# Kernel tuning notes

Hardware: AMD Instinct MI355X
Metric: run time of the kernel (lower is better)

The kernel has to match this reference:

```python
import jax, jax.numpy as jnp
import numpy as np

B, T, C, H = 4, 2048, 1024, 16
D = C // H  # head_size = 64


def _layernorm(x, g, b, eps=1e-5):
    mu = jnp.mean(x, axis=-1, keepdims=True)
    var = jnp.var(x, axis=-1, keepdims=True)
    return (x - mu) * jax.lax.rsqrt(var + eps) * g + b


def setup_inputs() -> dict:
    key = jax.random.key(0)
    ks = jax.random.split(key, 12)
    s = 0.02
    return {
        "x": jax.random.normal(ks[0], (B, T, C), dtype=jnp.float32),
        "Wq": jax.random.normal(ks[1], (C, C), dtype=jnp.float32) * s,
        "Wk": jax.random.normal(ks[2], (C, C), dtype=jnp.float32) * s,
        "Wv": jax.random.normal(ks[3], (C, C), dtype=jnp.float32) * s,
        "Wo": jax.random.normal(ks[4], (C, C), dtype=jnp.float32) * s,
        "bo": jnp.zeros((C,), dtype=jnp.float32),
        "ln1_g": jnp.ones((C,), dtype=jnp.float32),
        "ln1_b": jnp.zeros((C,), dtype=jnp.float32),
        "ln2_g": jnp.ones((C,), dtype=jnp.float32),
        "ln2_b": jnp.zeros((C,), dtype=jnp.float32),
        "W1": jax.random.normal(ks[5], (C, 4 * C), dtype=jnp.float32) * s,
        "b1": jnp.zeros((4 * C,), dtype=jnp.float32),
        "W2": jax.random.normal(ks[6], (4 * C, C), dtype=jnp.float32) * s,
        "b2": jnp.zeros((C,), dtype=jnp.float32),
    }


def reference(x, Wq, Wk, Wv, Wo, bo, ln1_g, ln1_b, ln2_g, ln2_b, W1, b1, W2, b2):
    # --- self-attention branch (pre-LN) ---
    h = _layernorm(x, ln1_g, ln1_b)
    q = (h @ Wq).reshape(B, T, H, D)
    k = (h @ Wk).reshape(B, T, H, D)
    v = (h @ Wv).reshape(B, T, H, D)
    scores = jnp.einsum("bqhd,bkhd->bhqk", q, k) * (D ** -0.5)
    causal = jnp.tril(jnp.ones((T, T), dtype=bool))
    scores = jnp.where(causal, scores, -jnp.inf)
    attn = jax.nn.softmax(scores, axis=-1)  # dropout=0 in eval
    out = jnp.einsum("bhqk,bkhd->bqhd", attn, v).reshape(B, T, C)
    x = x + (out @ Wo + bo)
    # --- feed-forward branch (pre-LN) ---
    h2 = _layernorm(x, ln2_g, ln2_b)
    ff = jax.nn.relu(h2 @ W1 + b1) @ W2 + b2
    return x + ff
```

## Files before the change

kernel.cpp:

```cpp
#include <hip/hip_runtime.h>
#include <hip/hip_bf16.h>
#include <math.h>

#define Bsz 4
#define Tsz 2048
#define Csz 1024
#define Hsz 16
#define Dsz 64
#define Msz (Bsz * Tsz)

typedef __attribute__((ext_vector_type(8))) __bf16 bf16x8;
typedef __attribute__((ext_vector_type(2))) __bf16 bf16x2;
typedef __attribute__((ext_vector_type(4))) float f32x4;

#define GLOBAL_AS __attribute__((address_space(1)))
#define LDS_AS    __attribute__((address_space(3)))


__device__ __forceinline__ float block_sum256(float v, float* sh) {
#pragma unroll
    for (int o = 32; o > 0; o >>= 1) v += __shfl_down(v, o, 64);
    int lane = threadIdx.x & 63, w = threadIdx.x >> 6;
    __syncthreads();
    if (lane == 0) sh[w] = v;
    __syncthreads();
    return sh[0] + sh[1] + sh[2] + sh[3];
}


__global__ __launch_bounds__(256) void layernorm_bf16(const float* __restrict__ x,
                                                      const float* __restrict__ g,
                                                      const float* __restrict__ b,
                                                      __bf16* __restrict__ out) {
    __shared__ float sh[4];
    const int row = blockIdx.x;
    const float* xr = x + (size_t)row * Csz;
    float v[4];
    float s = 0.f, ss = 0.f;
#pragma unroll
    for (int i = 0; i < 4; i++) {
        v[i] = xr[threadIdx.x + i * 256];
        s += v[i];
        ss += v[i] * v[i];
    }
    float tot = block_sum256(s, sh);
    float mean = tot * (1.0f / Csz);
    float tot2 = block_sum256(ss, sh);
    float var = tot2 * (1.0f / Csz) - mean * mean;
    float inv = rsqrtf(var + 1e-5f);
    __bf16* orow = out + (size_t)row * Csz;
#pragma unroll
    for (int i = 0; i < 4; i++) {
        int c = threadIdx.x + i * 256;
        orow[c] = (__bf16)((v[i] - mean) * inv * g[c] + b[c]);
    }
}


__global__ __launch_bounds__(256) void transpose_bf16(const float* __restrict__ W,
                                                      __bf16* __restrict__ Wt,
                                                      int K, int N) {
    __shared__ float t[32][33];
    const int k0 = blockIdx.y * 32, n0 = blockIdx.x * 32;
    const int c = threadIdx.x & 31, r8 = threadIdx.x >> 5;
#pragma unroll
    for (int it = 0; it < 4; it++) {
        int r = r8 + it * 8;
        t[r][c] = W[(size_t)(k0 + r) * N + n0 + c];
    }
    __syncthreads();
#pragma unroll
    for (int it = 0; it < 4; it++) {
        int r = r8 + it * 8;
        Wt[(size_t)(n0 + r) * K + k0 + c] = (__bf16)t[c][r];
    }
}

__global__ __launch_bounds__(256) void transpose4_bf16(const float* __restrict__ Wa,
                                                       const float* __restrict__ Wb,
                                                       const float* __restrict__ Wc,
                                                       const float* __restrict__ Wd,
                                                       __bf16* __restrict__ Ta,
                                                       __bf16* __restrict__ Tb,
                                                       __bf16* __restrict__ Tc,
                                                       __bf16* __restrict__ Td) {
    __shared__ float t[32][33];
    const float* W = (blockIdx.z == 0) ? Wa : (blockIdx.z == 1) ? Wb : (blockIdx.z == 2) ? Wc : Wd;
    __bf16* Wt = (blockIdx.z == 0) ? Ta : (blockIdx.z == 1) ? Tb : (blockIdx.z == 2) ? Tc : Td;
    const int k0 = blockIdx.y * 32, n0 = blockIdx.x * 32;
    const int c = threadIdx.x & 31, r8 = threadIdx.x >> 5;
#pragma unroll
    for (int it = 0; it < 4; it++) {
        int r = r8 + it * 8;
        t[r][c] = W[(size_t)(k0 + r) * Csz + n0 + c];
    }
    __syncthreads();
#pragma unroll
    for (int it = 0; it < 4; it++) {
        int r = r8 + it * 8;
        Wt[(size_t)(n0 + r) * Csz + k0 + c] = (__bf16)t[c][r];
    }
}


__global__ __launch_bounds__(256) void gemm_bf16(const __bf16* __restrict__ A,
                                                 const __bf16* __restrict__ Bt,
                                                 float* __restrict__ Cf,
                                                 float* __restrict__ Cf2,
                                                 __bf16* __restrict__ Cb,
                                                 int M, int N, int K, int ld,
                                                 const float* __restrict__ bias,
                                                 const float* __restrict__ resid,
                                                 int do_relu) {
    __shared__ __bf16 As[128 * 64];
    __shared__ __bf16 Bs[128 * 64];

    const int tid = threadIdx.x;
    const int lane = tid & 63;
    const int w = tid >> 6;
    const int rowBase = blockIdx.y * 128;
    const int colBase = blockIdx.x * 128;
    const int wr = (w & 1) * 64;
    const int wc = (w >> 1) * 64;

    const __bf16* Ak = A + (size_t)blockIdx.z * K;
    const __bf16* Bk = Bt + (size_t)blockIdx.z * K;
    float* Cfu = Cf;
    const float* residu = resid;
    const float* biasu = bias;
    if (blockIdx.z == 1) { Cfu = Cf2; residu = nullptr; biasu = nullptr; }

    const int m16 = lane & 15;
    const int kg = lane >> 4;
    const int swz = m16 & 7;

    const int sr = lane >> 3;
    const int sc = lane & 7;
    const int gcs = sc ^ sr;

    f32x4 acc[4][4] = {};

    for (int k0 = 0; k0 < K; k0 += 64) {
        __syncthreads();
#pragma unroll
        for (int it = 0; it < 4; it++) {
            int lr = w * 32 + it * 8;
            const __bf16* ga = Ak + (size_t)(rowBase + lr + sr) * ld + k0 + gcs * 8;
            __builtin_amdgcn_global_load_lds((const GLOBAL_AS unsigned int*)ga,
                                             (LDS_AS unsigned int*)(As + lr * 64),
                                             16, 0, 0);
            const __bf16* gb = Bk + (size_t)(colBase + lr + sr) * ld + k0 + gcs * 8;
            __builtin_amdgcn_global_load_lds((const GLOBAL_AS unsigned int*)gb,
                                             (LDS_AS unsigned int*)(Bs + lr * 64),
                                             16, 0, 0);
        }
        __syncthreads();

#pragma unroll
        for (int s = 0; s < 2; s++) {
            const int slot = ((s * 4 + kg) ^ swz) * 8;
            bf16x8 af[4], bfv[4];
#pragma unroll
            for (int i = 0; i < 4; i++)
                af[i] = *(const bf16x8*)(As + (wr + i * 16 + m16) * 64 + slot);
#pragma unroll
            for (int j = 0; j < 4; j++)
                bfv[j] = *(const bf16x8*)(Bs + (wc + j * 16 + m16) * 64 + slot);
#pragma unroll
            for (int i = 0; i < 4; i++)
#pragma unroll
                for (int j = 0; j < 4; j++)
                    acc[i][j] = __builtin_amdgcn_mfma_f32_16x16x32_bf16(af[i], bfv[j], acc[i][j], 0, 0, 0);
        }
    }

    const int cn = lane & 15;
    const int rq = (lane >> 4) * 4;
    float bj[4];
#pragma unroll
    for (int j = 0; j < 4; j++)
        bj[j] = biasu ? biasu[colBase + wc + j * 16 + cn] : 0.f;

#pragma unroll
    for (int i = 0; i < 4; i++) {
#pragma unroll
        for (int r = 0; r < 4; r++) {
            int m = rowBase + wr + i * 16 + rq + r;
            size_t rowOff = (size_t)m * N;
#pragma unroll
            for (int j = 0; j < 4; j++) {
                int n = colBase + wc + j * 16 + cn;
                float v = acc[i][j][r] + bj[j];
                if (do_relu) v = fmaxf(v, 0.f);
                if (residu) v += residu[rowOff + n];
                if (Cfu) Cfu[rowOff + n] = v;
                if (Cb && blockIdx.z == 0) Cb[rowOff + n] = (__bf16)v;
            }
        }
    }
}


__global__ __launch_bounds__(256) void add_partial(float* __restrict__ out,
                                                   const float* __restrict__ p,
                                                   const float* __restrict__ b2) {
    size_t i = ((size_t)blockIdx.x * 256 + threadIdx.x) * 4;
    float4 o = *(float4*)(out + i);
    const float4 a = *(const float4*)(p + i);
    const float4 bb = *(const float4*)(b2 + (i & (Csz - 1)));
    o.x += a.x + bb.x;
    o.y += a.y + bb.y;
    o.z += a.z + bb.z;
    o.w += a.w + bb.w;
    *(float4*)(out + i) = o;
}


__global__ __launch_bounds__(256, 4) void attn_mfma(const __bf16* __restrict__ QKV,
                                                    __bf16* __restrict__ O) {
    __shared__ __bf16 Ks[64 * 64];
    __shared__ __bf16 Vt[64 * 72];
    __shared__ __bf16 Ps[128 * 72];

    const int tid = threadIdx.x;
    const int lane = tid & 63;
    const int w = tid >> 6;
    const int bh = blockIdx.x;
    const int b = bh >> 4, h = bh & 15;
    const int qt = (int)gridDim.y - 1 - (int)blockIdx.y;
    const int qbase = qt * 128;
    const int ld3C = 3 * Csz;

    const __bf16* Qg = QKV + (size_t)(b * Tsz) * ld3C + h * Dsz;
    const __bf16* Kg = Qg + Csz;
    const __bf16* Vg = Qg + 2 * Csz;

    const int m16 = lane & 15;
    const int kg = lane >> 4;
    const int rq = kg * 4;
    const int wrow = w * 32;
    const int swz = m16 & 7;

    bf16x8 aq[2][2];
#pragma unroll
    for (int i = 0; i < 2; i++)
#pragma unroll
        for (int s = 0; s < 2; s++)
            aq[i][s] = *(const bf16x8*)(Qg + (size_t)(qbase + wrow + i * 16 + m16) * ld3C + (s * 4 + kg) * 8);

    const int sr = lane >> 3;
    const int sc = lane & 7;
    const int gcs = sc ^ sr;

    const int kp = (lane & 31) * 2;
    const int dg = w * 2 + (lane >> 5);

    f32x4 Oacc[2][4];
    float l_part[2][4];
#pragma unroll
    for (int i = 0; i < 2; i++)
#pragma unroll
        for (int j = 0; j < 4; j++) Oacc[i][j] = (f32x4){0.f, 0.f, 0.f, 0.f};
#pragma unroll
    for (int i = 0; i < 2; i++)
#pragma unroll
        for (int r = 0; r < 4; r++) l_part[i][r] = 0.f;

    const float CEXP = 0.18033688f;

    const int nkt = 2 * qt + 2;
    for (int kt = 0; kt < nkt; kt++) {
        const int kbase = kt * 64;
        __syncthreads();

#pragma unroll
        for (int it = 0; it < 2; it++) {
            int lr = w * 16 + it * 8 + sr;
            const __bf16* src = Kg + (size_t)(kbase + lr) * ld3C + gcs * 8;
            __builtin_amdgcn_global_load_lds((const GLOBAL_AS unsigned int*)src,
                                             (LDS_AS unsigned int*)(Ks + (w * 16 + it * 8) * 64),
                                             16, 0, 0);
        }
        bf16x8 v0 = *(const bf16x8*)(Vg + (size_t)(kbase + kp) * ld3C + dg * 8);
        bf16x8 v1 = *(const bf16x8*)(Vg + (size_t)(kbase + kp + 1) * ld3C + dg * 8);
        __syncthreads();

        f32x4 S[2][4];
#pragma unroll
        for (int i = 0; i < 2; i++)
#pragma unroll
            for (int j = 0; j < 4; j++) S[i][j] = (f32x4){0.f, 0.f, 0.f, 0.f};
#pragma unroll
        for (int s = 0; s < 2; s++) {
            bf16x8 bk[4];
#pragma unroll
            for (int j = 0; j < 4; j++)
                bk[j] = *(const bf16x8*)(Ks + (j * 16 + m16) * 64 + (((s * 4 + kg) ^ swz) * 8));
#pragma unroll
            for (int i = 0; i < 2; i++)
#pragma unroll
                for (int j = 0; j < 4; j++)
                    S[i][j] = __builtin_amdgcn_mfma_f32_16x16x32_bf16(aq[i][s], bk[j], S[i][j], 0, 0, 0);
        }

        const bool domask = (kt >= 2 * qt);
#pragma unroll
        for (int i = 0; i < 2; i++) {
#pragma unroll
            for (int j = 0; j < 4; j++) {
#pragma unroll
                for (int r = 0; r < 4; r++) {
                    float arg = S[i][j][r] * CEXP;
                    if (domask && (kbase + j * 16 + m16 > qbase + wrow + i * 16 + rq + r))
                        arg = -INFINITY;
                    float e = exp2f(arg);
                    S[i][j][r] = e;
                    l_part[i][r] += e;
                }
            }
        }

#pragma unroll
        for (int i = 0; i < 2; i++)
#pragma unroll
            for (int j = 0; j < 4; j++)
#pragma unroll
                for (int r = 0; r < 4; r++)
                    Ps[(wrow + i * 16 + rq + r) * 72 + j * 16 + m16] = (__bf16)S[i][j][r];
#pragma unroll
        for (int e = 0; e < 8; e++) {
            bf16x2 pr;
            pr[0] = v0[e];
            pr[1] = v1[e];
            *(bf16x2*)(Vt + (dg * 8 + e) * 72 + kp) = pr;
        }
        __syncthreads();

#pragma unroll
        for (int s = 0; s < 2; s++) {
            bf16x8 ap[2], bv[4];
#pragma unroll
            for (int i = 0; i < 2; i++)
                ap[i] = *(const bf16x8*)(Ps + (wrow + i * 16 + m16) * 72 + s * 32 + kg * 8);
#pragma unroll
            for (int j = 0; j < 4; j++)
                bv[j] = *(const bf16x8*)(Vt + (j * 16 + m16) * 72 + s * 32 + kg * 8);
#pragma unroll
            for (int i = 0; i < 2; i++)
#pragma unroll
                for (int j = 0; j < 4; j++)
                    Oacc[i][j] = __builtin_amdgcn_mfma_f32_16x16x32_bf16(ap[i], bv[j], Oacc[i][j], 0, 0, 0);
        }
    }

#pragma unroll
    for (int i = 0; i < 2; i++) {
#pragma unroll
        for (int r = 0; r < 4; r++) {
            float l = l_part[i][r];
#pragma unroll
            for (int msk = 1; msk < 16; msk <<= 1) l += __shfl_xor(l, msk, 64);
            const float inv = 1.0f / l;
            const int qrow = qbase + wrow + i * 16 + rq + r;
            __bf16* orow = O + (size_t)(b * Tsz + qrow) * Csz + h * Dsz;
#pragma unroll
            for (int j = 0; j < 4; j++)
                orow[j * 16 + m16] = (__bf16)(Oacc[i][j][r] * inv);
        }
    }
}


extern "C" void kernel_launch(void* const* d_in, const int* in_sizes, int n_in,
                              void* d_out, int out_size, void* d_ws, size_t ws_size,
                              hipStream_t stream) {
    const float* x     = (const float*)d_in[0];
    const float* Wq    = (const float*)d_in[1];
    const float* Wk    = (const float*)d_in[2];
    const float* Wv    = (const float*)d_in[3];
    const float* Wo    = (const float*)d_in[4];
    const float* bo    = (const float*)d_in[5];
    const float* ln1_g = (const float*)d_in[6];
    const float* ln1_b = (const float*)d_in[7];
    const float* ln2_g = (const float*)d_in[8];
    const float* ln2_b = (const float*)d_in[9];
    const float* W1    = (const float*)d_in[10];
    const float* b1    = (const float*)d_in[11];
    const float* W2    = (const float*)d_in[12];
    const float* b2    = (const float*)d_in[13];
    float* out = (float*)d_out;

    const size_t MB = 1u << 20;
    char* w = (char*)d_ws;
    __bf16* h    = (__bf16*)(w + 0);
    __bf16* Wqkv = (__bf16*)(w + 16 * MB);
    __bf16* Wot  = (__bf16*)(w + 22 * MB);
    __bf16* W1t  = (__bf16*)(w + 24 * MB);
    __bf16* W2t  = (__bf16*)(w + 32 * MB);
    __bf16* QKVb = (__bf16*)(w + 40 * MB);
    __bf16* AO   = (__bf16*)(w + 88 * MB);
    __bf16* ff1  = (__bf16*)(w + 40 * MB);
    float*  p1   = (float*)(w + 0);

    transpose4_bf16<<<dim3(32, 32, 4), 256, 0, stream>>>(Wq, Wk, Wv, Wo,
                                                         Wqkv, Wqkv + 1024 * 1024, Wqkv + 2048 * 1024, Wot);
    transpose_bf16<<<dim3(4 * Csz / 32, Csz / 32), 256, 0, stream>>>(W1, W1t, Csz, 4 * Csz);
    transpose_bf16<<<dim3(Csz / 32, 4 * Csz / 32), 256, 0, stream>>>(W2, W2t, 4 * Csz, Csz);

    layernorm_bf16<<<Msz, 256, 0, stream>>>(x, ln1_g, ln1_b, h);
    gemm_bf16<<<dim3(3 * Csz / 128, Msz / 128), 256, 0, stream>>>(
        h, Wqkv, nullptr, nullptr, QKVb, Msz, 3 * Csz, Csz, Csz, nullptr, nullptr, 0);
    attn_mfma<<<dim3(Bsz * Hsz, Tsz / 128), 256, 0, stream>>>(QKVb, AO);
    gemm_bf16<<<dim3(Csz / 128, Msz / 128), 256, 0, stream>>>(
        AO, Wot, out, nullptr, nullptr, Msz, Csz, Csz, Csz, bo, x, 0);

    layernorm_bf16<<<Msz, 256, 0, stream>>>(out, ln2_g, ln2_b, h);
    gemm_bf16<<<dim3(4 * Csz / 128, Msz / 128), 256, 0, stream>>>(
        h, W1t, nullptr, nullptr, ff1, Msz, 4 * Csz, Csz, Csz, b1, nullptr, 1);
    gemm_bf16<<<dim3(Csz / 128, Msz / 128, 2), 256, 0, stream>>>(
        ff1, W2t, out, p1, nullptr, Msz, Csz, 2 * Csz, 4 * Csz, nullptr, out, 0);
    add_partial<<<Msz * Csz / 1024, 256, 0, stream>>>(out, p1, b2);
}
```

Measured before the change: 570.1 us.

## Double-buffer K/V loads in attention, add GEMM tile swizzle and native exp2

The attention kernel now double-buffers its K tile in LDS and prefetches the next V tile into registers, so the global loads for the next key block overlap the current block's compute. This replaces the two __syncthreads per iteration with manual waitcnt plus barrier. The mask check is hoisted out of the loop for non-diagonal tiles, exp2 uses the native builtin, and MFMA sections are wrapped in setprio. The GEMM remaps workgroup IDs across 8 groups to change cache locality. Occupancy bounds drop from 4 to 3 blocks per CU to fit the extra LDS and registers. The second barrier no longer waits on vmcnt, and it is unclear whether all hazards are still covered.

Result: faster. 540.3 us (-5.2%).

```diff
diff --git a/kernel.cpp b/kernel.cpp
--- a/kernel.cpp
+++ b/kernel.cpp
@@ -15,6 +15,13 @@
 
 #define GLOBAL_AS __attribute__((address_space(1)))
 #define LDS_AS    __attribute__((address_space(3)))
+
+#if __has_builtin(__builtin_amdgcn_exp2f)
+#define EXP2F(x) __builtin_amdgcn_exp2f(x)
+#define HAVE_NATIVE_EXP2 1
+#else
+#define HAVE_NATIVE_EXP2 0
+#endif
 
 
 __device__ __forceinline__ float block_sum256(float v, float* sh) {
@@ -118,8 +125,15 @@
     const int tid = threadIdx.x;
     const int lane = tid & 63;
     const int w = tid >> 6;
-    const int rowBase = blockIdx.y * 128;
-    const int colBase = blockIdx.x * 128;
+
+    const int nwg = (int)(gridDim.x * gridDim.y);
+    const int did = (int)(blockIdx.y * gridDim.x + blockIdx.x);
+    const int work = ((nwg & 7) == 0) ? ((did & 7) * (nwg >> 3) + (did >> 3)) : did;
+    const int bx = work % (int)gridDim.x;
+    const int by = work / (int)gridDim.x;
+
+    const int rowBase = by * 128;
+    const int colBase = bx * 128;
     const int wr = (w & 1) * 64;
     const int wc = (w >> 1) * 64;
 
@@ -216,9 +230,9 @@
 }
 
 
-__global__ __launch_bounds__(256, 4) void attn_mfma(const __bf16* __restrict__ QKV,
+__global__ __launch_bounds__(256, 3) void attn_mfma(const __bf16* __restrict__ QKV,
                                                     __bf16* __restrict__ O) {
-    __shared__ __bf16 Ks[64 * 64];
+    __shared__ __bf16 Ks[2][64 * 64];
     __shared__ __bf16 Vt[64 * 72];
     __shared__ __bf16 Ps[128 * 72];
 
@@ -267,23 +281,41 @@
         for (int r = 0; r < 4; r++) l_part[i][r] = 0.f;
 
     const float CEXP = 0.18033688f;
-
     const int nkt = 2 * qt + 2;
+
+#pragma unroll
+    for (int it = 0; it < 2; it++) {
+        int lr = w * 16 + it * 8 + sr;
+        const __bf16* src = Kg + (size_t)lr * ld3C + gcs * 8;
+        __builtin_amdgcn_global_load_lds((const GLOBAL_AS unsigned int*)src,
+                                         (LDS_AS unsigned int*)(&Ks[0][(w * 16 + it * 8) * 64]),
+                                         16, 0, 0);
+    }
+    bf16x8 vc0 = *(const bf16x8*)(Vg + (size_t)kp * ld3C + dg * 8);
+    bf16x8 vc1 = *(const bf16x8*)(Vg + (size_t)(kp + 1) * ld3C + dg * 8);
+    bf16x8 vn0, vn1;
+
     for (int kt = 0; kt < nkt; kt++) {
+        const int cur = kt & 1;
         const int kbase = kt * 64;
-        __syncthreads();
-
-#pragma unroll
-        for (int it = 0; it < 2; it++) {
-            int lr = w * 16 + it * 8 + sr;
-            const __bf16* src = Kg + (size_t)(kbase + lr) * ld3C + gcs * 8;
-            __builtin_amdgcn_global_load_lds((const GLOBAL_AS unsigned int*)src,
-                                             (LDS_AS unsigned int*)(Ks + (w * 16 + it * 8) * 64),
-                                             16, 0, 0);
-        }
-        bf16x8 v0 = *(const bf16x8*)(Vg + (size_t)(kbase + kp) * ld3C + dg * 8);
-        bf16x8 v1 = *(const bf16x8*)(Vg + (size_t)(kbase + kp + 1) * ld3C + dg * 8);
-        __syncthreads();
+
+        if (kt + 1 < nkt) {
+            const int nb = kbase + 64;
+#pragma unroll
+            for (int it = 0; it < 2; it++) {
+                int lr = w * 16 + it * 8 + sr;
+                const __bf16* src = Kg + (size_t)(nb + lr) * ld3C + gcs * 8;
+                __builtin_amdgcn_global_load_lds((const GLOBAL_AS unsigned int*)src,
+                                                 (LDS_AS unsigned int*)(&Ks[cur ^ 1][(w * 16 + it * 8) * 64]),
+                                                 16, 0, 0);
+            }
+            vn0 = *(const bf16x8*)(Vg + (size_t)(nb + kp) * ld3C + dg * 8);
+            vn1 = *(const bf16x8*)(Vg + (size_t)(nb + kp + 1) * ld3C + dg * 8);
+            asm volatile("s_waitcnt vmcnt(4)" ::: "memory");
+        } else {
+            asm volatile("s_waitcnt vmcnt(0)" ::: "memory");
+        }
+        __builtin_amdgcn_s_barrier();
 
         f32x4 S[2][4];
 #pragma unroll
@@ -295,29 +327,50 @@
             bf16x8 bk[4];
 #pragma unroll
             for (int j = 0; j < 4; j++)
-                bk[j] = *(const bf16x8*)(Ks + (j * 16 + m16) * 64 + (((s * 4 + kg) ^ swz) * 8));
+                bk[j] = *(const bf16x8*)(&Ks[cur][(j * 16 + m16) * 64 + (((s * 4 + kg) ^ swz) * 8)]);
+            __builtin_amdgcn_s_setprio(1);
 #pragma unroll
             for (int i = 0; i < 2; i++)
 #pragma unroll
                 for (int j = 0; j < 4; j++)
                     S[i][j] = __builtin_amdgcn_mfma_f32_16x16x32_bf16(aq[i][s], bk[j], S[i][j], 0, 0, 0);
-        }
-
-        const bool domask = (kt >= 2 * qt);
-#pragma unroll
-        for (int i = 0; i < 2; i++) {
-#pragma unroll
-            for (int j = 0; j < 4; j++) {
-#pragma unroll
-                for (int r = 0; r < 4; r++) {
-                    float arg = S[i][j][r] * CEXP;
-                    if (domask && (kbase + j * 16 + m16 > qbase + wrow + i * 16 + rq + r))
-                        arg = -INFINITY;
-                    float e = exp2f(arg);
-                    S[i][j][r] = e;
-                    l_part[i][r] += e;
-                }
-            }
+            __builtin_amdgcn_s_setprio(0);
+        }
+
+        if (kt >= 2 * qt) {
+#pragma unroll
+            for (int i = 0; i < 2; i++)
+#pragma unroll
+                for (int j = 0; j < 4; j++)
+#pragma unroll
+                    for (int r = 0; r < 4; r++) {
+                        float arg = S[i][j][r] * CEXP;
+                        if (kbase + j * 16 + m16 > qbase + wrow + i * 16 + rq + r)
+                            arg = -INFINITY;
+#if HAVE_NATIVE_EXP2
+                        float e = EXP2F(arg);
+#else
+                        float e = __expf(arg * 0.6931472f);
+#endif
+                        S[i][j][r] = e;
+                        l_part[i][r] += e;
+                    }
+        } else {
+#pragma unroll
+            for (int i = 0; i < 2; i++)
+#pragma unroll
+                for (int j = 0; j < 4; j++)
+#pragma unroll
+                    for (int r = 0; r < 4; r++) {
+                        float arg = S[i][j][r] * CEXP;
+#if HAVE_NATIVE_EXP2
+                        float e = EXP2F(arg);
+#else
+                        float e = __expf(arg * 0.6931472f);
+#endif
+                        S[i][j][r] = e;
+                        l_part[i][r] += e;
+                    }
         }
 
 #pragma unroll
@@ -330,11 +383,12 @@
 #pragma unroll
         for (int e = 0; e < 8; e++) {
             bf16x2 pr;
-            pr[0] = v0[e];
-            pr[1] = v1[e];
+            pr[0] = vc0[e];
+            pr[1] = vc1[e];
             *(bf16x2*)(Vt + (dg * 8 + e) * 72 + kp) = pr;
         }
-        __syncthreads();
+        asm volatile("s_waitcnt lgkmcnt(0)" ::: "memory");
+        __builtin_amdgcn_s_barrier();
 
 #pragma unroll
         for (int s = 0; s < 2; s++) {
@@ -345,12 +399,16 @@
 #pragma unroll
             for (int j = 0; j < 4; j++)
                 bv[j] = *(const bf16x8*)(Vt + (j * 16 + m16) * 72 + s * 32 + kg * 8);
+            __builtin_amdgcn_s_setprio(1);
 #pragma unroll
             for (int i = 0; i < 2; i++)
 #pragma unroll
                 for (int j = 0; j < 4; j++)
                     Oacc[i][j] = __builtin_amdgcn_mfma_f32_16x16x32_bf16(ap[i], bv[j], Oacc[i][j], 0, 0, 0);
-        }
+            __builtin_amdgcn_s_setprio(0);
+        }
+
+        if (kt + 1 < nkt) { vc0 = vn0; vc1 = vn1; }
     }
 
 #pragma unroll
```
